# Performance work log

Hardware: AMD Instinct MI355X
Metric: run time of the kernel (lower is better)

## Reference

```python
import jax, jax.numpy as jnp
import numpy as np

HEADS = 8
DIM_HEAD = 64
C = 512              # in_channels == inner_dim = heads*dim_head
WIN = 7              # window size implied by rel_pos table (2*7-1 = 13)
EPS = 1e-5


def setup_inputs() -> dict:
    key = jax.random.key(0)
    ks = jax.random.split(key, 6)
    B = 2048
    inner = HEADS * DIM_HEAD
    x = jax.random.normal(ks[0], (B, C, WIN, WIN), dtype=jnp.float32)
    gamma = jnp.ones((C,), dtype=jnp.float32)
    beta = jnp.zeros((C,), dtype=jnp.float32)
    w_qkv = jax.random.normal(ks[1], (C, 3 * inner), dtype=jnp.float32) / np.sqrt(C)
    rel_table = jax.random.normal(ks[2], (2 * WIN - 1, 2 * WIN - 1, HEADS), dtype=jnp.float32)
    w_out = jax.random.normal(ks[3], (inner, C), dtype=jnp.float32) / np.sqrt(inner)
    b_out = jnp.zeros((C,), dtype=jnp.float32)
    return {"x": x, "gamma": gamma, "beta": beta, "w_qkv": w_qkv,
            "rel_table": rel_table, "w_out": w_out, "b_out": b_out}


def _rel_pos_bias(rel_table, H, W):
    # Swin-style additive bias: bias[h, i, j] = table[hi-hj+H-1, wi-wj+W-1, h]
    hh = jnp.arange(H)
    ww = jnp.arange(W)
    hi = jnp.repeat(hh, W)          # [N] row index of each flattened position
    wi = jnp.tile(ww, H)            # [N] col index
    dh = hi[:, None] - hi[None, :] + (H - 1)   # [N, N]
    dw = wi[:, None] - wi[None, :] + (W - 1)   # [N, N]
    bias = rel_table[dh, dw]        # [N, N, heads]
    return jnp.transpose(bias, (2, 0, 1))      # [heads, N, N]


def reference(x, gamma, beta, w_qkv, rel_table, w_out, b_out):
    B, Cc, H, W = x.shape
    N = H * W
    shortcut = x
    xs = jnp.transpose(x.reshape(B, Cc, N), (0, 2, 1))   # [B, N, C]
    # LayerNorm over channel dim
    mu = jnp.mean(xs, axis=-1, keepdims=True)
    var = jnp.var(xs, axis=-1, keepdims=True)
    xn = (xs - mu) * jax.lax.rsqrt(var + EPS) * gamma + beta
    qkv = xn @ w_qkv                                      # [B, N, 3*inner]
    q, k, v = jnp.split(qkv, 3, axis=-1)
    def heads(t):
        return jnp.transpose(t.reshape(B, N, HEADS, DIM_HEAD), (0, 2, 1, 3))  # [B,h,N,d]
    q, k, v = heads(q), heads(k), heads(v)
    scale = DIM_HEAD ** -0.5
    dots = jnp.einsum('bhnd,bhmd->bhnm', q, k) * scale   # [B,h,N,N]
    dots = dots + _rel_pos_bias(rel_table, H, W)[None]   # add Swin-style bias
    attn = jax.nn.softmax(dots, axis=-1)
    out = jnp.einsum('bhnm,bhmd->bhnd', attn, v)         # [B,h,N,d]
    out = jnp.transpose(out, (0, 2, 1, 3)).reshape(B, N, HEADS * DIM_HEAD)
    out = out @ w_out + b_out                            # [B, N, C]
    out = jnp.transpose(out, (0, 2, 1)).reshape(B, Cc, H, W)
    return out + shortcut
```

## Files before the change

### kernel.cpp

```cpp
#include <hip/hip_runtime.h>

#define BATCH 2048
#define CH 512
#define NTOK 49
#define NHEAD 8
#define DHEAD 64

typedef __attribute__((ext_vector_type(8))) short bf16x8;
typedef __attribute__((ext_vector_type(4))) float f32x4;

__device__ __forceinline__ ushort f2bf(float f) {
  union { float f; unsigned u; } v; v.f = f;
  unsigned r = v.u + 0x7fffu + ((v.u >> 16) & 1u);
  return (ushort)(r >> 16);
}

__device__ __forceinline__ float bf2f(ushort u) {
  union { unsigned u; float f; } v; v.u = ((unsigned)u) << 16;
  return v.f;
}

#define MFMA16(a, b, c) __builtin_amdgcn_mfma_f32_16x16x32_bf16((a), (b), (c), 0, 0, 0)

#define GLOAD_LDS16(gsrc, ldst)                                                  \
  __builtin_amdgcn_global_load_lds((const __attribute__((address_space(1))) void*)(gsrc), \
                                   (__attribute__((address_space(3))) void*)(ldst), 16, 0, 0)

__global__ void prep_kernel(const float* __restrict__ w_qkv, const float* __restrict__ w_out,
                            const float* __restrict__ rel, ushort* __restrict__ wqkvB,
                            ushort* __restrict__ woutF, float* __restrict__ biasP) {
  int tid = blockIdx.x * blockDim.x + threadIdx.x;
  int stride = gridDim.x * blockDim.x;
  for (int i = tid; i < 12 * 16 * 8 * 64 * 8; i += stride) {
    int j = i & 7, lane = (i >> 3) & 63, cbs = (i >> 9) & 7, kk = (i >> 12) & 15, nb = i >> 16;
    int o = nb * 128 + cbs * 16 + (lane & 15);
    int c = kk * 32 + (lane >> 4) * 8 + j;
    wqkvB[i] = f2bf(w_qkv[c * 1536 + o]);
  }
  for (int i = tid; i < 32 * 16 * 64 * 8; i += stride) {
    int j = i & 7, lane = (i >> 3) & 63, ks = (i >> 9) & 15, cb = i >> 13;
    int o = cb * 16 + (lane & 15);
    int c = ks * 32 + (lane >> 4) * 8 + j;
    woutF[i] = f2bf(w_out[c * 512 + o]);
  }
  for (int i = tid; i < NHEAD * 64 * 64; i += stride) {
    int h = i >> 12, n = (i >> 6) & 63, m = i & 63;
    float v = -1e30f;
    if (n < NTOK && m < NTOK) {
      int dh = n / 7 - m / 7 + 6;
      int dw = n % 7 - m % 7 + 6;
      v = rel[(dh * 13 + dw) * 8 + h];
    }
    biasP[i] = v;
  }
}

__global__ __launch_bounds__(256) void ln_kernel(const float* __restrict__ x,
                                                 const float* __restrict__ gamma,
                                                 const float* __restrict__ beta,
                                                 ushort* __restrict__ xnW) {
  int b = blockIdx.x;
  int t = threadIdx.x;
  __shared__ ushort xsb[CH][NTOK];
  __shared__ float muL[64], rsL[64];
  const float4* x4 = (const float4*)(x + (size_t)b * CH * NTOK);
  for (int i4 = t; i4 < CH * NTOK / 4; i4 += 256) {
    float4 v = x4[i4];
    int lf = i4 * 4;
#pragma unroll
    for (int e = 0; e < 4; e++) {
      int idx = lf + e;
      int c = idx / NTOK, n = idx - c * NTOK;
      xsb[c][n] = f2bf(((const float*)&v)[e]);
    }
  }
  __syncthreads();
  int row = t >> 2, sub = t & 3;
  float s = 0.f, s2 = 0.f;
  if (row < NTOK) {
    for (int c = sub; c < CH; c += 4) {
      float v = bf2f(xsb[c][row]);
      s += v;
      s2 += v * v;
    }
  }
  s += __shfl_xor(s, 1);
  s += __shfl_xor(s, 2);
  s2 += __shfl_xor(s2, 1);
  s2 += __shfl_xor(s2, 2);
  if (sub == 0 && row < NTOK) {
    float m = s * (1.f / CH);
    muL[row] = m;
    rsL[row] = rsqrtf(s2 * (1.f / CH) - m * m + 1e-5f);
  }
  __syncthreads();
  ushort* dst = xnW + (size_t)b * NTOK * CH;
  for (int i = t; i < NTOK * 64; i += 256) {
    int n = i >> 6, c0 = (i & 63) * 8;
    float mu = muL[n], rs = rsL[n];
    ushort tmp[8];
#pragma unroll
    for (int j = 0; j < 8; j++) {
      int c = c0 + j;
      tmp[j] = f2bf((bf2f(xsb[c][n]) - mu) * rs * gamma[c] + beta[c]);
    }
    *(uint4*)(dst + (size_t)n * CH + c0) = *(const uint4*)tmp;
  }
}

__global__ __launch_bounds__(256, 4) void qkv_gemm(const ushort* __restrict__ xnW,
                                                   const ushort* __restrict__ wqkvB,
                                                   ushort* __restrict__ qW,
                                                   ushort* __restrict__ kW,
                                                   ushort* __restrict__ vW) {
  int bid = blockIdx.x;
  int f = (bid & 7) * 1176 + (bid >> 3);
  int mb = f / 12, nb = f - mb * 12;
  int r0 = mb * 128;
  int t = threadIdx.x, lane = t & 63, w = t >> 6;
  int wm = w >> 1, wn = w & 1;

  __shared__ __align__(16) ushort lds[8704];

  const int arow = lane & 15, g = lane >> 4;
  int srow0 = w * 16 + (lane >> 2);
  int cL = lane & 3;
  const ushort* wBbase = wqkvB + (size_t)nb * 16 * 4096;
  const ushort* xbase = xnW + (size_t)r0 * CH;

#pragma unroll
  for (int i = 0; i < 2; i++) {
    int row = i * 64 + srow0;
    int cG = cL ^ ((row >> 1) & 3);
    GLOAD_LDS16(xbase + (size_t)row * CH + cG * 8, lds + (i * 64 + w * 16) * 32);
  }
  __syncthreads();

  f32x4 acc[4][4];
#pragma unroll
  for (int mt = 0; mt < 4; mt++)
#pragma unroll
    for (int nt = 0; nt < 4; nt++) acc[mt][nt] = (f32x4){0.f, 0.f, 0.f, 0.f};

  int cur = 0;
  for (int step = 0; step < 16; ++step) {
    const ushort* wp = wBbase + (size_t)step * 4096 + (wn * 4) * 512 + lane * 8;
    bf16x8 bfr[4];
#pragma unroll
    for (int nt = 0; nt < 4; nt++) bfr[nt] = *(const bf16x8*)(wp + nt * 512);
    if (step < 15) {
      int nxt = cur ^ 1, kk = step + 1;
#pragma unroll
      for (int i = 0; i < 2; i++) {
        int row = i * 64 + srow0;
        int cG = cL ^ ((row >> 1) & 3);
        GLOAD_LDS16(xbase + (size_t)row * CH + kk * 32 + cG * 8,
                    lds + nxt * 4096 + (i * 64 + w * 16) * 32);
      }
    }
    const ushort* lA = lds + cur * 4096;
    bf16x8 afr[4];
#pragma unroll
    for (int mt = 0; mt < 4; mt++) {
      int row = wm * 64 + mt * 16 + arow;
      afr[mt] = *(const bf16x8*)&lA[row * 32 + (g ^ ((row >> 1) & 3)) * 8];
    }
#pragma unroll
    for (int mt = 0; mt < 4; mt++)
#pragma unroll
      for (int nt = 0; nt < 4; nt++) acc[mt][nt] = MFMA16(afr[mt], bfr[nt], acc[mt][nt]);
    __syncthreads();
    cur ^= 1;
  }

  ushort(*oL)[136] = (ushort(*)[136])lds;
  int h0 = (nb & 3) * 2;
  int sct = nb >> 2;
#pragma unroll
  for (int hh = 0; hh < 2; hh++) {
    if (wm == hh) {
#pragma unroll
      for (int mt = 0; mt < 4; mt++)
#pragma unroll
        for (int nt = 0; nt < 4; nt++)
#pragma unroll
          for (int r = 0; r < 4; r++) {
            int rn = mt * 16 + 4 * g + r;
            oL[rn][wn * 64 + nt * 16 + arow] = f2bf(acc[mt][nt][r]);
          }
    }
    __syncthreads();
    if (sct < 2) {
      ushort* dst = (sct == 0 ? qW : kW);
      for (int i = t; i < 64 * 16; i += 256) {
        int rn = i >> 4, c8 = i & 15;
        int grow = r0 + hh * 64 + rn;
        int b = grow / 49, n = grow - b * 49;
        int h = h0 + (c8 >> 3);
        *(uint4*)(dst + (size_t)(b * 8 + h) * (NTOK * 64) + n * 64 + (c8 & 7) * 8) =
            *(const uint4*)&oL[rn][c8 * 8];
      }
    } else {
      for (int i = t; i < 64 * 128; i += 256) {
        int rn = i & 63, col = i >> 6;
        int grow = r0 + hh * 64 + rn;
        int b = grow / 49, n = grow - b * 49;
        int h = h0 + (col >> 6), d = col & 63;
        vW[(size_t)(b * 8 + h) * 4096 + d * 64 + n] = oL[rn][col];
      }
    }
    __syncthreads();
  }
}

__global__ __launch_bounds__(512, 4) void attn2(const ushort* __restrict__ qW,
                                                const ushort* __restrict__ kW,
                                                const ushort* __restrict__ vW,
                                                const float* __restrict__ biasP,
                                                ushort* __restrict__ aoW) {
  int b = blockIdx.x;
  int t = threadIdx.x;
  int lane = t & 63;
  int h = t >> 6;

  __shared__ ushort pL[8][64][72];
  ushort(*pl)[72] = pL[h];

  const int c = lane & 15, g = lane >> 4;
  const ushort* qb = qW + (size_t)(b * 8 + h) * NTOK * 64;
  const ushort* kb = kW + (size_t)(b * 8 + h) * NTOK * 64;
  const ushort* vb = vW + (size_t)(b * 8 + h) * 64 * 64;
  const float* bp = biasP + h * 64 * 64;

  f32x4 s[4][4];
#pragma unroll
  for (int mt = 0; mt < 4; mt++)
#pragma unroll
    for (int nt = 0; nt < 4; nt++) s[mt][nt] = (f32x4){0.f, 0.f, 0.f, 0.f};
#pragma unroll
  for (int ks = 0; ks < 2; ks++) {
    bf16x8 kf[4];
#pragma unroll
    for (int nt = 0; nt < 4; nt++)
      kf[nt] = *(const bf16x8*)(kb + (size_t)(nt * 16 + c) * 64 + ks * 32 + g * 8);
#pragma unroll
    for (int mt = 0; mt < 4; mt++) {
      bf16x8 qf = *(const bf16x8*)(qb + (size_t)(mt * 16 + c) * 64 + ks * 32 + g * 8);
#pragma unroll
      for (int nt = 0; nt < 4; nt++) s[mt][nt] = MFMA16(qf, kf[nt], s[mt][nt]);
    }
  }
#pragma unroll
  for (int mt = 0; mt < 4; mt++)
#pragma unroll
    for (int nt = 0; nt < 4; nt++)
#pragma unroll
      for (int r = 0; r < 4; r++) {
        int n = mt * 16 + 4 * g + r;
        int m = nt * 16 + c;
        s[mt][nt][r] = s[mt][nt][r] * 0.125f + bp[n * 64 + m];
      }

#pragma unroll
  for (int mt = 0; mt < 4; mt++)
#pragma unroll
    for (int r = 0; r < 4; r++) {
      float mx = fmaxf(fmaxf(s[mt][0][r], s[mt][1][r]), fmaxf(s[mt][2][r], s[mt][3][r]));
      mx = fmaxf(mx, __shfl_xor(mx, 1));
      mx = fmaxf(mx, __shfl_xor(mx, 2));
      mx = fmaxf(mx, __shfl_xor(mx, 4));
      mx = fmaxf(mx, __shfl_xor(mx, 8));
      float p0 = __expf(s[mt][0][r] - mx);
      float p1 = __expf(s[mt][1][r] - mx);
      float p2 = __expf(s[mt][2][r] - mx);
      float p3 = __expf(s[mt][3][r] - mx);
      float sum = p0 + p1 + p2 + p3;
      sum += __shfl_xor(sum, 1);
      sum += __shfl_xor(sum, 2);
      sum += __shfl_xor(sum, 4);
      sum += __shfl_xor(sum, 8);
      float rinv = 1.f / sum;
      int n = mt * 16 + 4 * g + r;
      pl[n][0 * 16 + c] = f2bf(p0 * rinv);
      pl[n][1 * 16 + c] = f2bf(p1 * rinv);
      pl[n][2 * 16 + c] = f2bf(p2 * rinv);
      pl[n][3 * 16 + c] = f2bf(p3 * rinv);
    }

  f32x4 o[4][4];
#pragma unroll
  for (int mt = 0; mt < 4; mt++)
#pragma unroll
    for (int nt = 0; nt < 4; nt++) o[mt][nt] = (f32x4){0.f, 0.f, 0.f, 0.f};
#pragma unroll
  for (int ks = 0; ks < 2; ks++) {
    bf16x8 vf[4];
#pragma unroll
    for (int nt = 0; nt < 4; nt++)
      vf[nt] = *(const bf16x8*)(vb + (size_t)(nt * 16 + c) * 64 + ks * 32 + g * 8);
#pragma unroll
    for (int mt = 0; mt < 4; mt++) {
      bf16x8 pf = *(const bf16x8*)&pl[mt * 16 + c][ks * 32 + g * 8];
#pragma unroll
      for (int nt = 0; nt < 4; nt++) o[mt][nt] = MFMA16(pf, vf[nt], o[mt][nt]);
    }
  }

#pragma unroll
  for (int mt = 0; mt < 4; mt++)
#pragma unroll
    for (int nt = 0; nt < 4; nt++)
#pragma unroll
      for (int r = 0; r < 4; r++) {
        int n = mt * 16 + 4 * g + r;
        pl[n][nt * 16 + c] = f2bf(o[mt][nt][r]);
      }
  ushort* ao = aoW + (size_t)b * NTOK * CH + h * 64;
  for (int i = lane; i < NTOK * 8; i += 64) {
    int row = i >> 3, c8 = i & 7;
    *(uint4*)(ao + (size_t)row * CH + c8 * 8) = *(const uint4*)&pl[row][c8 * 8];
  }
}

__global__ __launch_bounds__(256, 4) void proj_kernel(const ushort* __restrict__ aoW,
                                                      const ushort* __restrict__ woutF,
                                                      const float* __restrict__ b_out,
                                                      const float* __restrict__ x,
                                                      float* __restrict__ out) {
  int bid = blockIdx.x;
  int f = (bid & 7) * 512 + (bid >> 3);
  int mb = f >> 2, nbp = f & 3;
  int b0 = mb * 2;
  int t = threadIdx.x, lane = t & 63, w = t >> 6;
  int wm = w >> 1, wn = w & 1;

  __shared__ __align__(16) char ldsraw[33792];
  ushort* lds = (ushort*)ldsraw;
  float(*oL)[132] = (float(*)[132])ldsraw;

  for (int i = t; i < 2 * 30 * 32; i += 256) {
    int buf = i >= 960;
    int r2 = i - buf * 960;
    int rr = r2 >> 5;
    int row = (rr < 15) ? (49 + rr) : (98 + rr);
    lds[buf * 4096 + row * 32 + (i & 31)] = 0;
  }

  const int arow = lane & 15, g = lane >> 4;
  int srow0 = w * 16 + (lane >> 2);
  int cL = lane & 3;

  {
#pragma unroll
    for (int i = 0; i < 2; i++) {
      int row = i * 64 + srow0;
      int n = row & 63, bb = b0 + (row >> 6);
      int cG = cL ^ ((row >> 1) & 3);
      if (n < NTOK)
        GLOAD_LDS16(aoW + ((size_t)bb * NTOK + n) * CH + cG * 8, lds + (i * 64 + w * 16) * 32);
    }
  }
  __syncthreads();

  f32x4 acc[4][4];
#pragma unroll
  for (int mt = 0; mt < 4; mt++)
#pragma unroll
    for (int nt = 0; nt < 4; nt++) acc[mt][nt] = (f32x4){0.f, 0.f, 0.f, 0.f};

  int cur = 0;
  for (int step = 0; step < 16; ++step) {
    const ushort* wp = woutF + ((size_t)(nbp * 8 + wn * 4) * 16 + step) * 512 + lane * 8;
    bf16x8 bfr[4];
#pragma unroll
    for (int nt = 0; nt < 4; nt++) bfr[nt] = *(const bf16x8*)(wp + (size_t)nt * 16 * 512);
    if (step < 15) {
      int nxt = cur ^ 1, kk = step + 1;
#pragma unroll
      for (int i = 0; i < 2; i++) {
        int row = i * 64 + srow0;
        int n = row & 63, bb = b0 + (row >> 6);
        int cG = cL ^ ((row >> 1) & 3);
        if (n < NTOK)
          GLOAD_LDS16(aoW + ((size_t)bb * NTOK + n) * CH + kk * 32 + cG * 8,
                      lds + nxt * 4096 + (i * 64 + w * 16) * 32);
      }
    }
    const ushort* lA = lds + cur * 4096;
    bf16x8 afr[4];
#pragma unroll
    for (int mt = 0; mt < 4; mt++) {
      int row = wm * 64 + mt * 16 + arow;
      afr[mt] = *(const bf16x8*)&lA[row * 32 + (g ^ ((row >> 1) & 3)) * 8];
    }
#pragma unroll
    for (int mt = 0; mt < 4; mt++)
#pragma unroll
      for (int nt = 0; nt < 4; nt++) acc[mt][nt] = MFMA16(afr[mt], bfr[nt], acc[mt][nt]);
    __syncthreads();
    cur ^= 1;
  }

  const float* bo = b_out + nbp * 128;
#pragma unroll
  for (int hh = 0; hh < 2; hh++) {
    if (wm == hh) {
#pragma unroll
      for (int mt = 0; mt < 4; mt++)
#pragma unroll
        for (int nt = 0; nt < 4; nt++)
#pragma unroll
          for (int r = 0; r < 4; r++) {
            int rn = mt * 16 + 4 * g + r;
            if (rn < NTOK) oL[rn][wn * 64 + nt * 16 + arow] = acc[mt][nt][r];
          }
    }
    __syncthreads();
    int b = b0 + hh;
    const float4* x4 = (const float4*)(x + ((size_t)b * CH + nbp * 128) * NTOK);
    float4* o4 = (float4*)(out + ((size_t)b * CH + nbp * 128) * NTOK);
    for (int i = t; i < 1568; i += 256) {
      float4 xv = x4[i];
      float4 ov;
      int lf = i * 4;
#pragma unroll
      for (int e = 0; e < 4; e++) {
        int cl = (lf + e) / NTOK, n = (lf + e) - cl * NTOK;
        ((float*)&ov)[e] = oL[n][cl] + bo[cl] + ((const float*)&xv)[e];
      }
      o4[i] = ov;
    }
    __syncthreads();
  }
}

extern "C" void kernel_launch(void* const* d_in, const int* in_sizes, int n_in,
                              void* d_out, int out_size, void* d_ws, size_t ws_size,
                              hipStream_t stream) {
  const float* x = (const float*)d_in[0];
  const float* gamma = (const float*)d_in[1];
  const float* beta = (const float*)d_in[2];
  const float* w_qkv = (const float*)d_in[3];
  const float* rel = (const float*)d_in[4];
  const float* w_out = (const float*)d_in[5];
  const float* b_out = (const float*)d_in[6];
  float* out = (float*)d_out;

  char* ws = (char*)d_ws;
  size_t off = 0;
  ushort* wqkvB = (ushort*)(ws + off); off += (size_t)12 * 16 * 4096 * 2;
  ushort* woutF = (ushort*)(ws + off); off += (size_t)512 * 512 * 2;
  float* biasP = (float*)(ws + off);   off += (size_t)NHEAD * 64 * 64 * 4;
  ushort* qW = (ushort*)(ws + off);    off += ((size_t)BATCH * 8 * NTOK * 64 + 1024) * 2;
  ushort* kW = (ushort*)(ws + off);    off += ((size_t)BATCH * 8 * NTOK * 64 + 1024) * 2;
  ushort* vW = (ushort*)(ws + off);    off += (size_t)BATCH * 8 * 64 * 64 * 2;
  ushort* xnW = (ushort*)(ws + off);   off += (size_t)BATCH * NTOK * CH * 2;
  ushort* aoW = xnW;
  (void)ws_size;

  prep_kernel<<<1024, 256, 0, stream>>>(w_qkv, w_out, rel, wqkvB, woutF, biasP);
  ln_kernel<<<BATCH, 256, 0, stream>>>(x, gamma, beta, xnW);
  qkv_gemm<<<784 * 12, 256, 0, stream>>>(xnW, wqkvB, qW, kW, vW);
  attn2<<<BATCH, 512, 0, stream>>>(qW, kW, vW, biasP, aoW);
  proj_kernel<<<BATCH / 2 * 4, 256, 0, stream>>>(aoW, woutF, b_out, x, out);
}
```

Measured before the change: 617.9 us.

## Fuse attention with output projection and deepen QKV GEMM K-stage

The attention kernel now keeps each batch's per-head outputs in shared memory and performs the output projection, bias add and residual directly, removing the attention-output workspace round trip and the separate projection kernel launch. Each 512-thread block runs a 64x512x512 GEMM reading W_out from global or L2 without LDS staging. The QKV GEMM stages 64-wide K chunks with a new XOR swizzle, which halves the number of barriers and double-buffer swaps. The costs are a larger shared-memory footprint (72KB in attnproj, 32KB in qkv_gemm), which may lower occupancy, and repeated per-block streaming of W_out.

Result: faster. 589.2 us (-4.7%).

```diff
diff --git a/kernel.cpp b/kernel.cpp
--- a/kernel.cpp
+++ b/kernel.cpp
@@ -120,19 +120,20 @@
   int t = threadIdx.x, lane = t & 63, w = t >> 6;
   int wm = w >> 1, wn = w & 1;
 
-  __shared__ __align__(16) ushort lds[8704];
+  __shared__ __align__(16) ushort lds[16384];
 
   const int arow = lane & 15, g = lane >> 4;
-  int srow0 = w * 16 + (lane >> 2);
-  int cL = lane & 3;
   const ushort* wBbase = wqkvB + (size_t)nb * 16 * 4096;
   const ushort* xbase = xnW + (size_t)r0 * CH;
 
-#pragma unroll
-  for (int i = 0; i < 2; i++) {
-    int row = i * 64 + srow0;
-    int cG = cL ^ ((row >> 1) & 3);
-    GLOAD_LDS16(xbase + (size_t)row * CH + cG * 8, lds + (i * 64 + w * 16) * 32);
+  int drow = t >> 3;
+  int slot = t & 7;
+  int gchunk = slot ^ (drow & 7);
+
+#pragma unroll
+  for (int i = 0; i < 4; i++) {
+    int row = drow + i * 32;
+    GLOAD_LDS16(xbase + (size_t)row * CH + gchunk * 8, lds + i * 2048 + t * 8);
   }
   __syncthreads();
 
@@ -143,32 +144,34 @@
     for (int nt = 0; nt < 4; nt++) acc[mt][nt] = (f32x4){0.f, 0.f, 0.f, 0.f};
 
   int cur = 0;
-  for (int step = 0; step < 16; ++step) {
-    const ushort* wp = wBbase + (size_t)step * 4096 + (wn * 4) * 512 + lane * 8;
-    bf16x8 bfr[4];
-#pragma unroll
-    for (int nt = 0; nt < 4; nt++) bfr[nt] = *(const bf16x8*)(wp + nt * 512);
-    if (step < 15) {
-      int nxt = cur ^ 1, kk = step + 1;
-#pragma unroll
-      for (int i = 0; i < 2; i++) {
-        int row = i * 64 + srow0;
-        int cG = cL ^ ((row >> 1) & 3);
-        GLOAD_LDS16(xbase + (size_t)row * CH + kk * 32 + cG * 8,
-                    lds + nxt * 4096 + (i * 64 + w * 16) * 32);
-      }
-    }
-    const ushort* lA = lds + cur * 4096;
-    bf16x8 afr[4];
-#pragma unroll
-    for (int mt = 0; mt < 4; mt++) {
-      int row = wm * 64 + mt * 16 + arow;
-      afr[mt] = *(const bf16x8*)&lA[row * 32 + (g ^ ((row >> 1) & 3)) * 8];
-    }
-#pragma unroll
-    for (int mt = 0; mt < 4; mt++)
-#pragma unroll
-      for (int nt = 0; nt < 4; nt++) acc[mt][nt] = MFMA16(afr[mt], bfr[nt], acc[mt][nt]);
+  for (int stage = 0; stage < 8; ++stage) {
+    if (stage < 7) {
+      int nxt = cur ^ 1, kk = stage + 1;
+#pragma unroll
+      for (int i = 0; i < 4; i++) {
+        GLOAD_LDS16(xbase + (size_t)(drow + i * 32) * CH + kk * 64 + gchunk * 8,
+                    lds + nxt * 8192 + i * 2048 + t * 8);
+      }
+    }
+    const ushort* lA = lds + cur * 8192;
+#pragma unroll
+    for (int ks = 0; ks < 2; ks++) {
+      int kk2 = stage * 2 + ks;
+      const ushort* wp = wBbase + (size_t)kk2 * 4096 + (wn * 4) * 512 + lane * 8;
+      bf16x8 bfr[4];
+#pragma unroll
+      for (int nt = 0; nt < 4; nt++) bfr[nt] = *(const bf16x8*)(wp + nt * 512);
+      bf16x8 afr[4];
+#pragma unroll
+      for (int mt = 0; mt < 4; mt++) {
+        int row = wm * 64 + mt * 16 + arow;
+        afr[mt] = *(const bf16x8*)&lA[row * 64 + ((ks * 4 + g) ^ (arow & 7)) * 8];
+      }
+#pragma unroll
+      for (int mt = 0; mt < 4; mt++)
+#pragma unroll
+        for (int nt = 0; nt < 4; nt++) acc[mt][nt] = MFMA16(afr[mt], bfr[nt], acc[mt][nt]);
+    }
     __syncthreads();
     cur ^= 1;
   }
@@ -213,24 +216,27 @@
   }
 }
 
-__global__ __launch_bounds__(512, 4) void attn2(const ushort* __restrict__ qW,
+__global__ __launch_bounds__(512) void attnproj(const ushort* __restrict__ qW,
                                                 const ushort* __restrict__ kW,
                                                 const ushort* __restrict__ vW,
                                                 const float* __restrict__ biasP,
-                                                ushort* __restrict__ aoW) {
+                                                const ushort* __restrict__ woutF,
+                                                const float* __restrict__ b_out,
+                                                const float* __restrict__ x,
+                                                float* __restrict__ out) {
   int b = blockIdx.x;
   int t = threadIdx.x;
   int lane = t & 63;
-  int h = t >> 6;
-
-  __shared__ ushort pL[8][64][72];
-  ushort(*pl)[72] = pL[h];
+  int w = t >> 6;
+
+  __shared__ __align__(16) ushort lds[36864];
+  ushort(*pl)[72] = (ushort(*)[72])(lds + w * 4608);
 
   const int c = lane & 15, g = lane >> 4;
-  const ushort* qb = qW + (size_t)(b * 8 + h) * NTOK * 64;
-  const ushort* kb = kW + (size_t)(b * 8 + h) * NTOK * 64;
-  const ushort* vb = vW + (size_t)(b * 8 + h) * 64 * 64;
-  const float* bp = biasP + h * 64 * 64;
+  const ushort* qb = qW + (size_t)(b * 8 + w) * NTOK * 64;
+  const ushort* kb = kW + (size_t)(b * 8 + w) * NTOK * 64;
+  const ushort* vb = vW + (size_t)(b * 8 + w) * 64 * 64;
+  const float* bp = biasP + w * 64 * 64;
 
   f32x4 s[4][4];
 #pragma unroll
@@ -305,7 +311,9 @@
       for (int nt = 0; nt < 4; nt++) o[mt][nt] = MFMA16(pf, vf[nt], o[mt][nt]);
     }
   }
-
+  __syncthreads();
+
+  ushort(*aoL)[520] = (ushort(*)[520])lds;
 #pragma unroll
   for (int mt = 0; mt < 4; mt++)
 #pragma unroll
@@ -313,98 +321,36 @@
 #pragma unroll
       for (int r = 0; r < 4; r++) {
         int n = mt * 16 + 4 * g + r;
-        pl[n][nt * 16 + c] = f2bf(o[mt][nt][r]);
-      }
-  ushort* ao = aoW + (size_t)b * NTOK * CH + h * 64;
-  for (int i = lane; i < NTOK * 8; i += 64) {
-    int row = i >> 3, c8 = i & 7;
-    *(uint4*)(ao + (size_t)row * CH + c8 * 8) = *(const uint4*)&pl[row][c8 * 8];
-  }
-}
-
-__global__ __launch_bounds__(256, 4) void proj_kernel(const ushort* __restrict__ aoW,
-                                                      const ushort* __restrict__ woutF,
-                                                      const float* __restrict__ b_out,
-                                                      const float* __restrict__ x,
-                                                      float* __restrict__ out) {
-  int bid = blockIdx.x;
-  int f = (bid & 7) * 512 + (bid >> 3);
-  int mb = f >> 2, nbp = f & 3;
-  int b0 = mb * 2;
-  int t = threadIdx.x, lane = t & 63, w = t >> 6;
-  int wm = w >> 1, wn = w & 1;
-
-  __shared__ __align__(16) char ldsraw[33792];
-  ushort* lds = (ushort*)ldsraw;
-  float(*oL)[132] = (float(*)[132])ldsraw;
-
-  for (int i = t; i < 2 * 30 * 32; i += 256) {
-    int buf = i >= 960;
-    int r2 = i - buf * 960;
-    int rr = r2 >> 5;
-    int row = (rr < 15) ? (49 + rr) : (98 + rr);
-    lds[buf * 4096 + row * 32 + (i & 31)] = 0;
-  }
-
-  const int arow = lane & 15, g = lane >> 4;
-  int srow0 = w * 16 + (lane >> 2);
-  int cL = lane & 3;
-
-  {
-#pragma unroll
-    for (int i = 0; i < 2; i++) {
-      int row = i * 64 + srow0;
-      int n = row & 63, bb = b0 + (row >> 6);
-      int cG = cL ^ ((row >> 1) & 3);
-      if (n < NTOK)
-        GLOAD_LDS16(aoW + ((size_t)bb * NTOK + n) * CH + cG * 8, lds + (i * 64 + w * 16) * 32);
-    }
-  }
+        aoL[n][w * 64 + nt * 16 + c] = (n < NTOK) ? f2bf(o[mt][nt][r]) : (ushort)0;
+      }
   __syncthreads();
 
-  f32x4 acc[4][4];
-#pragma unroll
-  for (int mt = 0; mt < 4; mt++)
-#pragma unroll
-    for (int nt = 0; nt < 4; nt++) acc[mt][nt] = (f32x4){0.f, 0.f, 0.f, 0.f};
-
-  int cur = 0;
-  for (int step = 0; step < 16; ++step) {
-    const ushort* wp = woutF + ((size_t)(nbp * 8 + wn * 4) * 16 + step) * 512 + lane * 8;
+  f32x4 pacc[4][4];
+#pragma unroll
+  for (int mt = 0; mt < 4; mt++)
+#pragma unroll
+    for (int nt = 0; nt < 4; nt++) pacc[mt][nt] = (f32x4){0.f, 0.f, 0.f, 0.f};
+#pragma unroll 4
+  for (int step = 0; step < 16; step++) {
     bf16x8 bfr[4];
 #pragma unroll
-    for (int nt = 0; nt < 4; nt++) bfr[nt] = *(const bf16x8*)(wp + (size_t)nt * 16 * 512);
-    if (step < 15) {
-      int nxt = cur ^ 1, kk = step + 1;
-#pragma unroll
-      for (int i = 0; i < 2; i++) {
-        int row = i * 64 + srow0;
-        int n = row & 63, bb = b0 + (row >> 6);
-        int cG = cL ^ ((row >> 1) & 3);
-        if (n < NTOK)
-          GLOAD_LDS16(aoW + ((size_t)bb * NTOK + n) * CH + kk * 32 + cG * 8,
-                      lds + nxt * 4096 + (i * 64 + w * 16) * 32);
-      }
-    }
-    const ushort* lA = lds + cur * 4096;
+    for (int nt = 0; nt < 4; nt++)
+      bfr[nt] = *(const bf16x8*)(woutF + ((size_t)((w * 4 + nt) * 16 + step)) * 512 + lane * 8);
     bf16x8 afr[4];
 #pragma unroll
-    for (int mt = 0; mt < 4; mt++) {
-      int row = wm * 64 + mt * 16 + arow;
-      afr[mt] = *(const bf16x8*)&lA[row * 32 + (g ^ ((row >> 1) & 3)) * 8];
-    }
-#pragma unroll
     for (int mt = 0; mt < 4; mt++)
-#pragma unroll
-      for (int nt = 0; nt < 4; nt++) acc[mt][nt] = MFMA16(afr[mt], bfr[nt], acc[mt][nt]);
+      afr[mt] = *(const bf16x8*)&aoL[mt * 16 + c][step * 32 + g * 8];
+#pragma unroll
+    for (int mt = 0; mt < 4; mt++)
+#pragma unroll
+      for (int nt = 0; nt < 4; nt++) pacc[mt][nt] = MFMA16(afr[mt], bfr[nt], pacc[mt][nt]);
+  }
+
+  float(*oL)[260] = (float(*)[260])lds;
+  for (int half = 0; half < 2; half++) {
     __syncthreads();
-    cur ^= 1;
-  }
-
-  const float* bo = b_out + nbp * 128;
-#pragma unroll
-  for (int hh = 0; hh < 2; hh++) {
-    if (wm == hh) {
+    if ((w >> 2) == half) {
+      int wl = w & 3;
 #pragma unroll
       for (int mt = 0; mt < 4; mt++)
 #pragma unroll
@@ -412,14 +358,15 @@
 #pragma unroll
           for (int r = 0; r < 4; r++) {
             int rn = mt * 16 + 4 * g + r;
-            if (rn < NTOK) oL[rn][wn * 64 + nt * 16 + arow] = acc[mt][nt][r];
+            if (rn < NTOK) oL[rn][wl * 64 + nt * 16 + c] = pacc[mt][nt][r];
           }
     }
     __syncthreads();
-    int b = b0 + hh;
-    const float4* x4 = (const float4*)(x + ((size_t)b * CH + nbp * 128) * NTOK);
-    float4* o4 = (float4*)(out + ((size_t)b * CH + nbp * 128) * NTOK);
-    for (int i = t; i < 1568; i += 256) {
+    int c0 = half * 256;
+    const float4* x4 = (const float4*)(x + ((size_t)b * CH + c0) * NTOK);
+    float4* o4 = (float4*)(out + ((size_t)b * CH + c0) * NTOK);
+    const float* bo = b_out + c0;
+    for (int i = t; i < 3136; i += 512) {
       float4 xv = x4[i];
       float4 ov;
       int lf = i * 4;
@@ -430,7 +377,6 @@
       }
       o4[i] = ov;
     }
-    __syncthreads();
   }
 }
 
@@ -455,12 +401,10 @@
   ushort* kW = (ushort*)(ws + off);    off += ((size_t)BATCH * 8 * NTOK * 64 + 1024) * 2;
   ushort* vW = (ushort*)(ws + off);    off += (size_t)BATCH * 8 * 64 * 64 * 2;
   ushort* xnW = (ushort*)(ws + off);   off += (size_t)BATCH * NTOK * CH * 2;
-  ushort* aoW = xnW;
   (void)ws_size;
 
   prep_kernel<<<1024, 256, 0, stream>>>(w_qkv, w_out, rel, wqkvB, woutF, biasP);
   ln_kernel<<<BATCH, 256, 0, stream>>>(x, gamma, beta, xnW);
   qkv_gemm<<<784 * 12, 256, 0, stream>>>(xnW, wqkvB, qW, kW, vW);
-  attn2<<<BATCH, 512, 0, stream>>>(qW, kW, vW, biasP, aoW);
-  proj_kernel<<<BATCH / 2 * 4, 256, 0, stream>>>(aoW, woutF, b_out, x, out);
-}
+  attnproj<<<BATCH, 512, 0, stream>>>(qW, kW, vW, biasP, woutF, b_out, x, out);
+}
```
